# Kernel tuning notes

Measured on AMD Instinct MI355X. Metric: run time of the kernel, lower is better.

## Reference

```python
import jax, jax.numpy as jnp
import numpy as np

DIM = 768
NUM_HEADS = 12
HEAD_DIM = DIM // NUM_HEADS
SCALE = HEAD_DIM ** -0.5
NUM_EXPERTS = 8
RANK = 16
ALPHA = 32
TOPK = 2
SCALING = ALPHA / RANK
B, S = 8, 1024


def setup_inputs() -> dict:
    key = jax.random.key(0)
    ks = jax.random.split(key, 12)
    d, e, r = DIM, NUM_EXPERTS, RANK
    inp = {
        "x": jax.random.normal(ks[0], (B, S, d), jnp.float32),
        # router gating network: Linear(d, E)
        "Wg": jax.random.normal(ks[1], (e, d), jnp.float32) * 0.02,
        "bg": jax.random.normal(ks[2], (e,), jnp.float32) * 0.02,
        # frozen qkv: Linear(d, 3d)
        "Wqkv": jax.random.normal(ks[3], (3 * d, d), jnp.float32) * 0.02,
        "bqkv": jax.random.normal(ks[4], (3 * d,), jnp.float32) * 0.02,
        # frozen proj: Linear(d, d)
        "Wproj": jax.random.normal(ks[5], (d, d), jnp.float32) * 0.02,
        "bproj": jax.random.normal(ks[6], (d,), jnp.float32) * 0.02,
        # stacked LoRA experts: A: Linear(d, r), Bm: Linear(r, 3d)
        "A": jax.random.normal(ks[7], (e, r, d), jnp.float32) * 0.05,
        "ba": jax.random.normal(ks[8], (e, r), jnp.float32) * 0.02,
        "Bm": jax.random.normal(ks[9], (e, 3 * d, r), jnp.float32) * 0.05,
        "bb": jax.random.normal(ks[10], (e, 3 * d), jnp.float32) * 0.02,
    }
    return inp


def reference(x, Wg, bg, Wqkv, bqkv, Wproj, bproj, A, ba, Bm, bb):
    b, s, d = x.shape
    t = b * s
    xf = x.reshape(t, d)

    # --- Router: softmax then top-k (topk of probs == topk of logits here) ---
    probs = jax.nn.softmax(xf @ Wg.T + bg, axis=-1)          # [T, E]
    top_w, top_idx = jax.lax.top_k(probs, TOPK)               # [T, k]
    # combine weights: combine[t, e] = sum_k top_w[t,k] * (top_idx[t,k]==e)
    combine = jnp.zeros((t, NUM_EXPERTS), x.dtype).at[
        jnp.arange(t)[:, None], top_idx].add(top_w)           # [T, E]

    # --- LoRA MoE delta (dense-equivalent of gather/scatter dispatch) ---
    h = jnp.einsum('td,erd->ter', xf, A) + ba                 # [T, E, r] (tiny)
    hw = h * combine[:, :, None]                              # weight tokens per expert
    delta = jnp.einsum('ter,eor->to', hw, Bm) + combine @ bb  # [T, 3d]
    delta = delta * SCALING

    # --- attention with LoRA-augmented qkv ---
    qkv = (xf @ Wqkv.T + bqkv) + delta                        # [T, 3d]
    qkv = qkv.reshape(b, s, 3, NUM_HEADS, HEAD_DIM)
    qkv = jnp.transpose(qkv, (2, 0, 3, 1, 4))                 # [3, B, H, S, hd]
    q, k, v = qkv[0], qkv[1], qkv[2]
    attn = jax.nn.softmax(jnp.einsum('bhsd,bhtd->bhst', q, k) * SCALE, axis=-1)
    out = jnp.einsum('bhst,bhtd->bhsd', attn, v)              # [B, H, S, hd]
    out = jnp.transpose(out, (0, 2, 1, 3)).reshape(b, s, d)
    return out @ Wproj.T + bproj
```

## Files before the change

kernel.cpp:

```cpp
#include <hip/hip_runtime.h>

#define TOK   8192
#define DIMD  768
#define NH    12
#define HD    64
#define NE    8
#define RK    16
#define O3    2304
#define KSIDE 192
#define KQKV  960
#define SCALING_F 2.0f
#define SM_SCALE 0.125f
#define PSTR  40

typedef short  short8  __attribute__((ext_vector_type(8)));
typedef ushort ushort8 __attribute__((ext_vector_type(8)));
typedef float  f32x4   __attribute__((ext_vector_type(4)));

__device__ __forceinline__ ushort f2bf_rn(float f) {
    union { float f; uint u; } v; v.f = f;
    uint r = (v.u + 0x7FFFu + ((v.u >> 16) & 1u)) >> 16;
    return (ushort)r;
}
__device__ __forceinline__ void split_bf(float f, ushort& hi, ushort& lo) {
    hi = f2bf_rn(f);
    union { uint u; float f; } h; h.u = (uint)hi << 16;
    lo = f2bf_rn(f - h.f);
}

__global__ __launch_bounds__(64) void router_kernel(
    const float* __restrict__ x, const float* __restrict__ Wg,
    const float* __restrict__ bg, float* __restrict__ topw, int* __restrict__ topidx)
{
    int t = blockIdx.x;
    int lane = threadIdx.x;
    const float* xr = x + (size_t)t * DIMD;
    float part[NE];
#pragma unroll
    for (int e = 0; e < NE; ++e) part[e] = 0.f;
#pragma unroll
    for (int i = 0; i < DIMD / 64; ++i) {
        int d = i * 64 + lane;
        float xv = xr[d];
#pragma unroll
        for (int e = 0; e < NE; ++e) part[e] += xv * Wg[e * DIMD + d];
    }
#pragma unroll
    for (int e = 0; e < NE; ++e) {
        float v = part[e];
#pragma unroll
        for (int off = 32; off > 0; off >>= 1) v += __shfl_xor(v, off);
        part[e] = v;
    }
    if (lane == 0) {
        float lg[NE], p[NE];
        float mx = -1e30f;
#pragma unroll
        for (int e = 0; e < NE; ++e) { lg[e] = part[e] + bg[e]; mx = fmaxf(mx, lg[e]); }
        float sum = 0.f;
#pragma unroll
        for (int e = 0; e < NE; ++e) { p[e] = __expf(lg[e] - mx); sum += p[e]; }
        float inv = 1.f / sum;
#pragma unroll
        for (int e = 0; e < NE; ++e) p[e] *= inv;
        int i0 = 0;
#pragma unroll
        for (int e = 1; e < NE; ++e) if (p[e] > p[i0]) i0 = e;
        int i1 = (i0 == 0) ? 1 : 0;
#pragma unroll
        for (int e = 0; e < NE; ++e) if (e != i0 && p[e] > p[i1]) i1 = e;
        topw[t * 2 + 0] = p[i0];
        topw[t * 2 + 1] = p[i1];
        topidx[t * 2 + 0] = i0;
        topidx[t * 2 + 1] = i1;
    }
}

__global__ __launch_bounds__(256) void lora_h_kernel(
    const float* __restrict__ x, const float* __restrict__ A, const float* __restrict__ ba,
    const float* __restrict__ topw, const int* __restrict__ topidx,
    float* __restrict__ hw2)
{
    __shared__ float xs[DIMD];
    int t = blockIdx.x;
    int tid = threadIdx.x;
    const float* xr = x + (size_t)t * DIMD;
    for (int i = tid; i < DIMD; i += 256) xs[i] = xr[i];
    __syncthreads();
    int outi = tid >> 3;
    int sub  = tid & 7;
    int k = outi >> 4;
    int r = outi & 15;
    int e = topidx[t * 2 + k];
    float w = topw[t * 2 + k];
    const float* Ar = A + ((size_t)e * RK + r) * DIMD;
    float s = 0.f;
    for (int d = sub; d < DIMD; d += 8) s += xs[d] * Ar[d];
    s += __shfl_xor(s, 1);
    s += __shfl_xor(s, 2);
    s += __shfl_xor(s, 4);
    if (sub == 0) hw2[t * 32 + outi] = w * (s + ba[e * RK + r]);
}

__global__ __launch_bounds__(64) void build_xside(
    const float* __restrict__ hw2, const float* __restrict__ topw,
    const int* __restrict__ topidx, float* __restrict__ xside)
{
    int t = blockIdx.x;
    int tid = threadIdx.x;
    float* xr = xside + (size_t)t * KSIDE;
    for (int i = tid; i < KSIDE; i += 64) xr[i] = 0.f;
    __syncthreads();
    if (tid < 32) {
        int k = tid >> 4, r = tid & 15;
        int e = topidx[t * 2 + k];
        xr[e * 16 + r] = hw2[t * 32 + tid];
    } else if (tid < 34) {
        int k = tid - 32;
        xr[128 + topidx[t * 2 + k]] = topw[t * 2 + k];
    }
}

__global__ __launch_bounds__(192) void build_wside(
    const float* __restrict__ Bm, const float* __restrict__ bb, float* __restrict__ wside)
{
    int o = blockIdx.x;
    int c = threadIdx.x;
    float v;
    if (c < 128) {
        int e = c >> 4, r = c & 15;
        v = SCALING_F * Bm[((size_t)e * O3 + o) * RK + r];
    } else if (c < 136) {
        v = SCALING_F * bb[(c - 128) * O3 + o];
    } else {
        v = 0.f;
    }
    wside[(size_t)o * KSIDE + c] = v;
}

__global__ __launch_bounds__(256) void convert_x(
    const float* __restrict__ x, const float* __restrict__ xside,
    ushort* __restrict__ Xh, ushort* __restrict__ Xl)
{
    int idx = blockIdx.x * 256 + threadIdx.x;
    int row = idx / (KQKV / 8);
    int cp  = idx % (KQKV / 8);
    int c = cp * 8;
    const float* src = (c < DIMD) ? (x + (size_t)row * DIMD + c)
                                  : (xside + (size_t)row * KSIDE + (c - DIMD));
    float4 v0 = *(const float4*)src;
    float4 v1 = *(const float4*)(src + 4);
    float vv[8] = {v0.x, v0.y, v0.z, v0.w, v1.x, v1.y, v1.z, v1.w};
    ushort8 h, l;
#pragma unroll
    for (int i = 0; i < 8; ++i) { ushort hh, ll; split_bf(vv[i], hh, ll); h[i] = hh; l[i] = ll; }
    *(ushort8*)(Xh + (size_t)row * KQKV + c) = h;
    *(ushort8*)(Xl + (size_t)row * KQKV + c) = l;
}

__global__ __launch_bounds__(256) void convert_wqkv(
    const float* __restrict__ Wqkv, const float* __restrict__ wside,
    ushort* __restrict__ Wh, ushort* __restrict__ Wl)
{
    int idx = blockIdx.x * 256 + threadIdx.x;
    int row = idx / (KQKV / 8);
    int cp  = idx % (KQKV / 8);
    int c = cp * 8;
    const float* src = (c < DIMD) ? (Wqkv + (size_t)row * DIMD + c)
                                  : (wside + (size_t)row * KSIDE + (c - DIMD));
    float4 v0 = *(const float4*)src;
    float4 v1 = *(const float4*)(src + 4);
    float vv[8] = {v0.x, v0.y, v0.z, v0.w, v1.x, v1.y, v1.z, v1.w};
    ushort8 h, l;
#pragma unroll
    for (int i = 0; i < 8; ++i) { ushort hh, ll; split_bf(vv[i], hh, ll); h[i] = hh; l[i] = ll; }
    *(ushort8*)(Wh + (size_t)row * KQKV + c) = h;
    *(ushort8*)(Wl + (size_t)row * KQKV + c) = l;
}

__global__ __launch_bounds__(256) void convert_wproj(
    const float* __restrict__ Wp, ushort* __restrict__ Wh, ushort* __restrict__ Wl)
{
    int idx = blockIdx.x * 256 + threadIdx.x;
    int c = idx * 8;
    float4 v0 = *(const float4*)(Wp + c);
    float4 v1 = *(const float4*)(Wp + c + 4);
    float vv[8] = {v0.x, v0.y, v0.z, v0.w, v1.x, v1.y, v1.z, v1.w};
    ushort8 h, l;
#pragma unroll
    for (int i = 0; i < 8; ++i) { ushort hh, ll; split_bf(vv[i], hh, ll); h[i] = hh; l[i] = ll; }
    *(ushort8*)(Wh + c) = h;
    *(ushort8*)(Wl + c) = l;
}


#define GEMM_CORE(Ahg, Alg, Bhg, Blg, K)                                          \
    __shared__ __align__(16) ushort Ah[128 * 64];                                 \
    __shared__ __align__(16) ushort Al[128 * 64];                                 \
    __shared__ __align__(16) ushort Bh[128 * 64];                                 \
    __shared__ __align__(16) ushort Bl[128 * 64];                                 \
    const int tid = threadIdx.x;                                                  \
    const int w = tid >> 6, l = tid & 63;                                         \
    const int lr = l & 15, lk = l >> 4;                                           \
    const int wm = w >> 1, wn = w & 1;                                            \
    const int row0 = blockIdx.y * 128, col0 = blockIdx.x * 128;                   \
    f32x4 acc[4][4];                                                              \
    _Pragma("unroll")                                                             \
    for (int m = 0; m < 4; ++m)                                                   \
        _Pragma("unroll")                                                         \
        for (int n = 0; n < 4; ++n) acc[m][n] = (f32x4)(0.f);                     \
    for (int kk = 0; kk < K; kk += 64) {                                          \
        __syncthreads();                                                          \
        _Pragma("unroll")                                                         \
        for (int i = 0; i < 4; ++i) {                                             \
            int q = i * 256 + tid;                                                \
            int row = q >> 3, s = q & 7;                                          \
            int chk = s ^ (row & 7);                                              \
            *(float4*)&Ah[row * 64 + s * 8] =                                     \
                *(const float4*)(Ahg + (size_t)(row0 + row) * K + kk + chk * 8);  \
            *(float4*)&Al[row * 64 + s * 8] =                                     \
                *(const float4*)(Alg + (size_t)(row0 + row) * K + kk + chk * 8);  \
            *(float4*)&Bh[row * 64 + s * 8] =                                     \
                *(const float4*)(Bhg + (size_t)(col0 + row) * K + kk + chk * 8);  \
            *(float4*)&Bl[row * 64 + s * 8] =                                     \
                *(const float4*)(Blg + (size_t)(col0 + row) * K + kk + chk * 8);  \
        }                                                                         \
        __syncthreads();                                                          \
        _Pragma("unroll")                                                         \
        for (int kh = 0; kh < 2; ++kh) {                                          \
            const int slot = (kh * 4 + lk) ^ (lr & 7);                            \
            short8 af[4], alf[4], bfr[4], blf[4];                                 \
            _Pragma("unroll")                                                     \
            for (int m = 0; m < 4; ++m) {                                         \
                int r = wm * 64 + m * 16 + lr;                                    \
                af[m]  = *(const short8*)&Ah[r * 64 + slot * 8];                  \
                alf[m] = *(const short8*)&Al[r * 64 + slot * 8];                  \
            }                                                                     \
            _Pragma("unroll")                                                     \
            for (int n = 0; n < 4; ++n) {                                         \
                int r = wn * 64 + n * 16 + lr;                                    \
                bfr[n] = *(const short8*)&Bh[r * 64 + slot * 8];                  \
                blf[n] = *(const short8*)&Bl[r * 64 + slot * 8];                  \
            }                                                                     \
            _Pragma("unroll")                                                     \
            for (int m = 0; m < 4; ++m)                                           \
                _Pragma("unroll")                                                 \
                for (int n = 0; n < 4; ++n)                                       \
                    acc[m][n] = __builtin_amdgcn_mfma_f32_16x16x32_bf16(af[m], bfr[n], acc[m][n], 0, 0, 0); \
            _Pragma("unroll")                                                     \
            for (int m = 0; m < 4; ++m)                                           \
                _Pragma("unroll")                                                 \
                for (int n = 0; n < 4; ++n)                                       \
                    acc[m][n] = __builtin_amdgcn_mfma_f32_16x16x32_bf16(alf[m], bfr[n], acc[m][n], 0, 0, 0); \
            _Pragma("unroll")                                                     \
            for (int m = 0; m < 4; ++m)                                           \
                _Pragma("unroll")                                                 \
                for (int n = 0; n < 4; ++n)                                       \
                    acc[m][n] = __builtin_amdgcn_mfma_f32_16x16x32_bf16(af[m], blf[n], acc[m][n], 0, 0, 0); \
        }                                                                         \
    }

__global__ __launch_bounds__(256) void gemm_qkv(
    const ushort* __restrict__ Ahg, const ushort* __restrict__ Alg,
    const ushort* __restrict__ Bhg, const ushort* __restrict__ Blg,
    const float* __restrict__ bias,
    ushort* __restrict__ Qb, ushort* __restrict__ Kb, ushort* __restrict__ Vtb)
{
    GEMM_CORE(Ahg, Alg, Bhg, Blg, KQKV)
#pragma unroll
    for (int n = 0; n < 4; ++n) {
        int ccb = col0 + wn * 64 + n * 16;
        int which = ccb / DIMD;
        int rem = ccb - which * DIMD;
        int h = rem >> 6;
        int d = (rem & 63) + lr;
        float bv = bias[ccb + lr];
#pragma unroll
        for (int m = 0; m < 4; ++m) {
#pragma unroll
            for (int j = 0; j < 4; ++j) {
                int rr = row0 + wm * 64 + m * 16 + lk * 4 + j;
                int b = rr >> 10, s = rr & 1023;
                int bh = b * NH + h;
                float v = acc[m][n][j] + bv;
                if (which == 0)
                    Qb[((size_t)bh * 1024 + s) * 64 + d] = f2bf_rn(v * SM_SCALE);
                else if (which == 1)
                    Kb[((size_t)bh * 1024 + s) * 64 + d] = f2bf_rn(v);
                else
                    Vtb[((size_t)bh * 64 + d) * 1024 + s] = f2bf_rn(v);
            }
        }
    }
}

__global__ __launch_bounds__(256) void gemm_proj(
    const ushort* __restrict__ Ahg, const ushort* __restrict__ Alg,
    const ushort* __restrict__ Bhg, const ushort* __restrict__ Blg,
    const float* __restrict__ bias, float* __restrict__ C, int N)
{
    GEMM_CORE(Ahg, Alg, Bhg, Blg, DIMD)
#pragma unroll
    for (int n = 0; n < 4; ++n) {
        int cc = col0 + wn * 64 + n * 16 + lr;
        float bv = bias[cc];
#pragma unroll
        for (int m = 0; m < 4; ++m) {
#pragma unroll
            for (int j = 0; j < 4; ++j) {
                int rr = row0 + wm * 64 + m * 16 + lk * 4 + j;
                C[(size_t)rr * N + cc] = acc[m][n][j] + bv;
            }
        }
    }
}

__global__ __launch_bounds__(256) void attn_mfma(
    const ushort* __restrict__ Qb, const ushort* __restrict__ Kb,
    const ushort* __restrict__ Vtb,
    ushort* __restrict__ Oh, ushort* __restrict__ Ol)
{
    __shared__ __align__(16) ushort Ksh[32 * 64];
    __shared__ __align__(16) ushort Vsh[64 * PSTR];
    __shared__ __align__(16) ushort Psh[4][16 * PSTR];
    const int tid = threadIdx.x;
    const int wv = tid >> 6, l = tid & 63;
    const int lr = l & 15, g = l >> 4;
    const int bh = blockIdx.y;
    const int qt = blockIdx.x;
    const int q0 = qt * 64 + wv * 16;

    short8 qA0, qA1;
    {
        const ushort* qp = Qb + ((size_t)bh * 1024 + q0 + lr) * 64 + g * 8;
        qA0 = *(const short8*)(qp);
        qA1 = *(const short8*)(qp + 32);
    }
    f32x4 oacc[4];
#pragma unroll
    for (int i = 0; i < 4; ++i) oacc[i] = (f32x4)(0.f);
    float lp[4] = {0.f, 0.f, 0.f, 0.f};

    const int skey = tid >> 3, scol = tid & 7;
    const int sslot = scol ^ (skey & 7);
    const ushort* kg = Kb + ((size_t)bh * 1024 + skey) * 64 + scol * 8;
    const int vd = tid >> 2, vko = (tid & 3) * 8;
    const ushort* vg = Vtb + ((size_t)bh * 64 + vd) * 1024 + vko;
    ushort* pbase = &Psh[wv][0];
    const int cx = (g ^ (lr & 7)) * 8;
    const int cy = ((4 + g) ^ (lr & 7)) * 8;

    for (int k0 = 0; k0 < 1024; k0 += 32) {
        __syncthreads();
        *(short8*)&Ksh[skey * 64 + sslot * 8] = *(const short8*)(kg + (size_t)k0 * 64);
        *(short8*)&Vsh[vd * PSTR + vko] = *(const short8*)(vg + k0);
        __syncthreads();

        f32x4 s0 = (f32x4)(0.f), s1 = (f32x4)(0.f);
        {
            short8 kf00 = *(const short8*)&Ksh[lr * 64 + cx];
            short8 kf10 = *(const short8*)&Ksh[(16 + lr) * 64 + cx];
            short8 kf01 = *(const short8*)&Ksh[lr * 64 + cy];
            short8 kf11 = *(const short8*)&Ksh[(16 + lr) * 64 + cy];
            s0 = __builtin_amdgcn_mfma_f32_16x16x32_bf16(qA0, kf00, s0, 0, 0, 0);
            s1 = __builtin_amdgcn_mfma_f32_16x16x32_bf16(qA0, kf10, s1, 0, 0, 0);
            s0 = __builtin_amdgcn_mfma_f32_16x16x32_bf16(qA1, kf01, s0, 0, 0, 0);
            s1 = __builtin_amdgcn_mfma_f32_16x16x32_bf16(qA1, kf11, s1, 0, 0, 0);
        }
#pragma unroll
        for (int r = 0; r < 4; ++r) {
            float p0 = __expf(s0[r]);
            float p1 = __expf(s1[r]);
            lp[r] += p0 + p1;
            pbase[(g * 4 + r) * PSTR + lr] = f2bf_rn(p0);
            pbase[(g * 4 + r) * PSTR + 16 + lr] = f2bf_rn(p1);
        }
        short8 pA = *(const short8*)&pbase[lr * PSTR + g * 8];
#pragma unroll
        for (int dt = 0; dt < 4; ++dt) {
            short8 vB = *(const short8*)&Vsh[(dt * 16 + lr) * PSTR + g * 8];
            oacc[dt] = __builtin_amdgcn_mfma_f32_16x16x32_bf16(pA, vB, oacc[dt], 0, 0, 0);
        }
    }
#pragma unroll
    for (int r = 0; r < 4; ++r) {
        float v = lp[r];
        v += __shfl_xor(v, 1);
        v += __shfl_xor(v, 2);
        v += __shfl_xor(v, 4);
        v += __shfl_xor(v, 8);
        lp[r] = 1.f / v;
    }
    const int b = bh / NH, h = bh - b * NH;
    const int tbase = b * 1024 + q0;
#pragma unroll
    for (int dt = 0; dt < 4; ++dt) {
        int d = dt * 16 + lr;
#pragma unroll
        for (int r = 0; r < 4; ++r) {
            float v = oacc[dt][r] * lp[r];
            ushort hh, ll;
            split_bf(v, hh, ll);
            size_t off = (size_t)(tbase + g * 4 + r) * DIMD + h * HD + d;
            Oh[off] = hh;
            Ol[off] = ll;
        }
    }
}

extern "C" void kernel_launch(void* const* d_in, const int* in_sizes, int n_in,
                              void* d_out, int out_size, void* d_ws, size_t ws_size,
                              hipStream_t stream)
{
    const float* x     = (const float*)d_in[0];
    const float* Wg    = (const float*)d_in[1];
    const float* bg    = (const float*)d_in[2];
    const float* Wqkv  = (const float*)d_in[3];
    const float* bqkv  = (const float*)d_in[4];
    const float* Wproj = (const float*)d_in[5];
    const float* bproj = (const float*)d_in[6];
    const float* A     = (const float*)d_in[7];
    const float* ba    = (const float*)d_in[8];
    const float* Bm    = (const float*)d_in[9];
    const float* bb    = (const float*)d_in[10];
    float* out = (float*)d_out;

    char* w = (char*)d_ws;
    float*  topw   = (float*)w;   w += sizeof(float) * TOK * 2;
    int*    topidx = (int*)w;     w += sizeof(int) * TOK * 2;
    float*  hw2    = (float*)w;   w += sizeof(float) * TOK * 32;
    float*  xside  = (float*)w;   w += sizeof(float) * (size_t)TOK * KSIDE;
    float*  wside  = (float*)w;   w += sizeof(float) * (size_t)O3 * KSIDE;
    ushort* Xh     = (ushort*)w;  w += sizeof(ushort) * (size_t)TOK * KQKV;
    ushort* Xl     = (ushort*)w;  w += sizeof(ushort) * (size_t)TOK * KQKV;
    ushort* Whq    = (ushort*)w;  w += sizeof(ushort) * (size_t)O3 * KQKV;
    ushort* Wlq    = (ushort*)w;  w += sizeof(ushort) * (size_t)O3 * KQKV;
    ushort* Qb     = (ushort*)w;  w += sizeof(ushort) * (size_t)TOK * DIMD;
    ushort* Kb     = (ushort*)w;  w += sizeof(ushort) * (size_t)TOK * DIMD;
    ushort* Vtb    = (ushort*)w;  w += sizeof(ushort) * (size_t)TOK * DIMD;
    ushort* Wph    = (ushort*)w;  w += sizeof(ushort) * (size_t)DIMD * DIMD;
    ushort* Wpl    = (ushort*)w;  w += sizeof(ushort) * (size_t)DIMD * DIMD;
    ushort* Oh     = Xh;
    ushort* Ol     = Xl;

    router_kernel<<<TOK, 64, 0, stream>>>(x, Wg, bg, topw, topidx);
    lora_h_kernel<<<TOK, 256, 0, stream>>>(x, A, ba, topw, topidx, hw2);
    build_xside<<<TOK, 64, 0, stream>>>(hw2, topw, topidx, xside);
    build_wside<<<O3, 192, 0, stream>>>(Bm, bb, wside);
    convert_x<<<(TOK * (KQKV / 8)) / 256, 256, 0, stream>>>(x, xside, Xh, Xl);
    convert_wqkv<<<(O3 * (KQKV / 8)) / 256, 256, 0, stream>>>(Wqkv, wside, Whq, Wlq);
    convert_wproj<<<(DIMD * DIMD / 8) / 256, 256, 0, stream>>>(Wproj, Wph, Wpl);

    gemm_qkv<<<dim3(O3 / 128, TOK / 128), 256, 0, stream>>>(
        Xh, Xl, Whq, Wlq, bqkv, Qb, Kb, Vtb);
    attn_mfma<<<dim3(16, NH * 8), 256, 0, stream>>>(Qb, Kb, Vtb, Oh, Ol);
    gemm_proj<<<dim3(DIMD / 128, TOK / 128), 256, 0, stream>>>(
        Oh, Ol, Wph, Wpl, bproj, out, DIMD);
}
```

Before: 392.3 us.

## Drop low-part of weight split in QKV GEMM and swizzle block order

After: 373.2 us. 4.9% less time.

```diff
diff --git a/kernel.cpp b/kernel.cpp
--- a/kernel.cpp
+++ b/kernel.cpp
@@ -160,7 +160,7 @@
 
 __global__ __launch_bounds__(256) void convert_wqkv(
     const float* __restrict__ Wqkv, const float* __restrict__ wside,
-    ushort* __restrict__ Wh, ushort* __restrict__ Wl)
+    ushort* __restrict__ Wh)
 {
     int idx = blockIdx.x * 256 + threadIdx.x;
     int row = idx / (KQKV / 8);
@@ -171,11 +171,10 @@
     float4 v0 = *(const float4*)src;
     float4 v1 = *(const float4*)(src + 4);
     float vv[8] = {v0.x, v0.y, v0.z, v0.w, v1.x, v1.y, v1.z, v1.w};
-    ushort8 h, l;
-#pragma unroll
-    for (int i = 0; i < 8; ++i) { ushort hh, ll; split_bf(vv[i], hh, ll); h[i] = hh; l[i] = ll; }
+    ushort8 h;
+#pragma unroll
+    for (int i = 0; i < 8; ++i) h[i] = f2bf_rn(vv[i]);
     *(ushort8*)(Wh + (size_t)row * KQKV + c) = h;
-    *(ushort8*)(Wl + (size_t)row * KQKV + c) = l;
 }
 
 __global__ __launch_bounds__(256) void convert_wproj(
@@ -194,16 +193,80 @@
 }
 
 
-#define GEMM_CORE(Ahg, Alg, Bhg, Blg, K)                                          \
+#define GEMM_PROLOG                                                               \
+    const int tid = threadIdx.x;                                                  \
+    const int w = tid >> 6, l = tid & 63;                                         \
+    const int lr = l & 15, lk = l >> 4;                                           \
+    const int wm = w >> 1, wn = w & 1;                                            \
+    int bx, by;                                                                   \
+    {                                                                             \
+        int nx = gridDim.x;                                                       \
+        int nwg = nx * gridDim.y;                                                 \
+        int lin = blockIdx.y * nx + blockIdx.x;                                   \
+        int swz = (lin & 7) * (nwg >> 3) + (lin >> 3);                            \
+        bx = swz % nx; by = swz / nx;                                             \
+    }                                                                             \
+    const int row0 = by * 128, col0 = bx * 128;
+
+#define GEMM_CORE2(Ahg, Alg, Bhg, K)                                              \
+    __shared__ __align__(16) ushort Ah[128 * 64];                                 \
+    __shared__ __align__(16) ushort Al[128 * 64];                                 \
+    __shared__ __align__(16) ushort Bh[128 * 64];                                 \
+    GEMM_PROLOG                                                                   \
+    f32x4 acc[4][4];                                                              \
+    _Pragma("unroll")                                                             \
+    for (int m = 0; m < 4; ++m)                                                   \
+        _Pragma("unroll")                                                         \
+        for (int n = 0; n < 4; ++n) acc[m][n] = (f32x4)(0.f);                     \
+    for (int kk = 0; kk < K; kk += 64) {                                          \
+        __syncthreads();                                                          \
+        _Pragma("unroll")                                                         \
+        for (int i = 0; i < 4; ++i) {                                             \
+            int q = i * 256 + tid;                                                \
+            int row = q >> 3, s = q & 7;                                          \
+            int chk = s ^ (row & 7);                                              \
+            *(float4*)&Ah[row * 64 + s * 8] =                                     \
+                *(const float4*)(Ahg + (size_t)(row0 + row) * K + kk + chk * 8);  \
+            *(float4*)&Al[row * 64 + s * 8] =                                     \
+                *(const float4*)(Alg + (size_t)(row0 + row) * K + kk + chk * 8);  \
+            *(float4*)&Bh[row * 64 + s * 8] =                                     \
+                *(const float4*)(Bhg + (size_t)(col0 + row) * K + kk + chk * 8);  \
+        }                                                                         \
+        __syncthreads();                                                          \
+        _Pragma("unroll")                                                         \
+        for (int kh = 0; kh < 2; ++kh) {                                          \
+            const int slot = (kh * 4 + lk) ^ (lr & 7);                            \
+            short8 af[4], alf[4], bfr[4];                                         \
+            _Pragma("unroll")                                                     \
+            for (int m = 0; m < 4; ++m) {                                         \
+                int r = wm * 64 + m * 16 + lr;                                    \
+                af[m]  = *(const short8*)&Ah[r * 64 + slot * 8];                  \
+                alf[m] = *(const short8*)&Al[r * 64 + slot * 8];                  \
+            }                                                                     \
+            _Pragma("unroll")                                                     \
+            for (int n = 0; n < 4; ++n) {                                         \
+                int r = wn * 64 + n * 16 + lr;                                    \
+                bfr[n] = *(const short8*)&Bh[r * 64 + slot * 8];                  \
+            }                                                                     \
+            _Pragma("unroll")                                                     \
+            for (int m = 0; m < 4; ++m)                                           \
+                _Pragma("unroll")                                                 \
+                for (int n = 0; n < 4; ++n)                                       \
+                    acc[m][n] = __builtin_amdgcn_mfma_f32_16x16x32_bf16(af[m], bfr[n], acc[m][n], 0, 0, 0); \
+            _Pragma("unroll")                                                     \
+            for (int m = 0; m < 4; ++m)                                           \
+                _Pragma("unroll")                                                 \
+                for (int n = 0; n < 4; ++n)                                       \
+                    acc[m][n] = __builtin_amdgcn_mfma_f32_16x16x32_bf16(alf[m], bfr[n], acc[m][n], 0, 0, 0); \
+        }                                                                         \
+    }
+
+#define GEMM_CORE3(Ahg, Alg, Bhg, Blg, K)                                         \
     __shared__ __align__(16) ushort Ah[128 * 64];                                 \
     __shared__ __align__(16) ushort Al[128 * 64];                                 \
     __shared__ __align__(16) ushort Bh[128 * 64];                                 \
     __shared__ __align__(16) ushort Bl[128 * 64];                                 \
-    const int tid = threadIdx.x;                                                  \
-    const int w = tid >> 6, l = tid & 63;                                         \
-    const int lr = l & 15, lk = l >> 4;                                           \
-    const int wm = w >> 1, wn = w & 1;                                            \
-    const int row0 = blockIdx.y * 128, col0 = blockIdx.x * 128;                   \
+    GEMM_PROLOG                                                                   \
     f32x4 acc[4][4];                                                              \
     _Pragma("unroll")                                                             \
     for (int m = 0; m < 4; ++m)                                                   \
@@ -262,11 +325,11 @@
 
 __global__ __launch_bounds__(256) void gemm_qkv(
     const ushort* __restrict__ Ahg, const ushort* __restrict__ Alg,
-    const ushort* __restrict__ Bhg, const ushort* __restrict__ Blg,
+    const ushort* __restrict__ Bhg,
     const float* __restrict__ bias,
     ushort* __restrict__ Qb, ushort* __restrict__ Kb, ushort* __restrict__ Vtb)
 {
-    GEMM_CORE(Ahg, Alg, Bhg, Blg, KQKV)
+    GEMM_CORE2(Ahg, Alg, Bhg, KQKV)
 #pragma unroll
     for (int n = 0; n < 4; ++n) {
         int ccb = col0 + wn * 64 + n * 16;
@@ -299,7 +362,7 @@
     const ushort* __restrict__ Bhg, const ushort* __restrict__ Blg,
     const float* __restrict__ bias, float* __restrict__ C, int N)
 {
-    GEMM_CORE(Ahg, Alg, Bhg, Blg, DIMD)
+    GEMM_CORE3(Ahg, Alg, Bhg, Blg, DIMD)
 #pragma unroll
     for (int n = 0; n < 4; ++n) {
         int cc = col0 + wn * 64 + n * 16 + lr;
@@ -434,7 +497,6 @@
     ushort* Xh     = (ushort*)w;  w += sizeof(ushort) * (size_t)TOK * KQKV;
     ushort* Xl     = (ushort*)w;  w += sizeof(ushort) * (size_t)TOK * KQKV;
     ushort* Whq    = (ushort*)w;  w += sizeof(ushort) * (size_t)O3 * KQKV;
-    ushort* Wlq    = (ushort*)w;  w += sizeof(ushort) * (size_t)O3 * KQKV;
     ushort* Qb     = (ushort*)w;  w += sizeof(ushort) * (size_t)TOK * DIMD;
     ushort* Kb     = (ushort*)w;  w += sizeof(ushort) * (size_t)TOK * DIMD;
     ushort* Vtb    = (ushort*)w;  w += sizeof(ushort) * (size_t)TOK * DIMD;
@@ -448,11 +510,11 @@
     build_xside<<<TOK, 64, 0, stream>>>(hw2, topw, topidx, xside);
     build_wside<<<O3, 192, 0, stream>>>(Bm, bb, wside);
     convert_x<<<(TOK * (KQKV / 8)) / 256, 256, 0, stream>>>(x, xside, Xh, Xl);
-    convert_wqkv<<<(O3 * (KQKV / 8)) / 256, 256, 0, stream>>>(Wqkv, wside, Whq, Wlq);
+    convert_wqkv<<<(O3 * (KQKV / 8)) / 256, 256, 0, stream>>>(Wqkv, wside, Whq);
     convert_wproj<<<(DIMD * DIMD / 8) / 256, 256, 0, stream>>>(Wproj, Wph, Wpl);
 
     gemm_qkv<<<dim3(O3 / 128, TOK / 128), 256, 0, stream>>>(
-        Xh, Xl, Whq, Wlq, bqkv, Qb, Kb, Vtb);
+        Xh, Xl, Whq, bqkv, Qb, Kb, Vtb);
     attn_mfma<<<dim3(16, NH * 8), 256, 0, stream>>>(Qb, Kb, Vtb, Oh, Ol);
     gemm_proj<<<dim3(DIMD / 128, TOK / 128), 256, 0, stream>>>(
         Oh, Ol, Wph, Wpl, bproj, out, DIMD);
```
